# Kernel optimization log

Hardware: AMD Instinct MI355X
Metric: run time of the kernel (lower is better)

Reference implementation:

```python
import jax, jax.numpy as jnp
import numpy as np

NUM_HEADS = 16
HEAD_SIZE = 64
N_EMBD = 1024
BLOCK_SIZE = 2048
B, T = 4, 2048


def setup_inputs() -> dict:
    key = jax.random.key(0)
    ks = jax.random.split(key, 6)
    scale = (N_EMBD * NUM_HEADS) ** (-0.5)
    x = jax.random.normal(ks[0], (B, T, N_EMBD), dtype=jnp.float32)
    Wk = jax.random.normal(ks[1], (NUM_HEADS, N_EMBD, HEAD_SIZE), dtype=jnp.float32) * scale
    Wq = jax.random.normal(ks[2], (NUM_HEADS, N_EMBD, HEAD_SIZE), dtype=jnp.float32) * scale
    Wv = jax.random.normal(ks[3], (NUM_HEADS, N_EMBD, HEAD_SIZE), dtype=jnp.float32) * scale
    proj_w = jax.random.normal(ks[4], (N_EMBD, N_EMBD), dtype=jnp.float32) * (N_EMBD ** -0.5)
    proj_b = jax.random.normal(ks[5], (N_EMBD,), dtype=jnp.float32) * 0.01
    return {"x": x, "Wk": Wk, "Wq": Wq, "Wv": Wv, "proj_w": proj_w, "proj_b": proj_b}


def reference(x, Wk, Wq, Wv, proj_w, proj_b):
    Bsz, Tlen, C = x.shape
    # per-head projections: x [b,t,c] @ W [h,c,d] -> [b,h,t,d]
    q = jnp.einsum('btc,hcd->bhtd', x, Wq)
    k = jnp.einsum('btc,hcd->bhtd', x, Wk)
    v = jnp.einsum('btc,hcd->bhtd', x, Wv)
    wei = jnp.einsum('bhtd,bhsd->bhts', q, k) * (HEAD_SIZE ** -0.5)
    causal = jnp.tril(jnp.ones((Tlen, Tlen), dtype=bool))  # [T,T]
    wei = jnp.where(causal[None, None, :, :], wei, -jnp.inf)
    wei = jax.nn.softmax(wei, axis=-1)
    out = jnp.einsum('bhts,bhsd->bhtd', wei, v)
    out = out.transpose(0, 2, 1, 3).reshape(Bsz, Tlen, NUM_HEADS * HEAD_SIZE)
    out = out @ proj_w.T + proj_b  # nn.Linear: x W^T + b
    return out
```

## Files before the change

kernel.cpp:

```cpp
#include <hip/hip_runtime.h>
#include <hip/hip_bf16.h>

#define BB 4
#define TT 2048
#define CC 1024
#define HH 16
#define DD 64
#define MM (BB * TT)
#define NN_QKV 3072

typedef __attribute__((ext_vector_type(8))) short short8;
typedef __attribute__((ext_vector_type(4))) short short4v;
typedef __attribute__((ext_vector_type(4))) int i32x4;
typedef __attribute__((ext_vector_type(4))) float f32x4;
typedef __attribute__((ext_vector_type(16))) float f32x16;

static __device__ __forceinline__ float exp2_hw(float x) {
  return __builtin_amdgcn_exp2f(x);
}

static __device__ __forceinline__ short f2bf(float f) {
  __hip_bfloat16 h = __float2bfloat16(f);
  short s;
  __builtin_memcpy(&s, &h, 2);
  return s;
}

static __device__ __forceinline__ unsigned int pack2(float a, float b) {
  unsigned int lo = (unsigned short)f2bf(a);
  unsigned int hi = (unsigned short)f2bf(b);
  return lo | (hi << 16);
}

static __device__ __forceinline__ f32x16 zero16() {
  f32x16 z;
#pragma unroll
  for (int i = 0; i < 16; ++i) z[i] = 0.f;
  return z;
}

static __device__ __forceinline__ int swzv(int d) {
  return (((d & 7) ^ ((d >> 3) & 7)) << 4);
}

static __device__ __forceinline__ void gld16(const void* g, void* l) {
  __builtin_amdgcn_global_load_lds(
      (const __attribute__((address_space(1))) unsigned int*)g,
      (__attribute__((address_space(3))) unsigned int*)l, 16, 0, 0);
}

__global__ __launch_bounds__(256) void cvt8_kernel(const float* __restrict__ in,
                                                   short* __restrict__ out, int n8) {
  int i = blockIdx.x * 256 + threadIdx.x;
  if (i >= n8) return;
  const float4 a = ((const float4*)in)[i * 2];
  const float4 b = ((const float4*)in)[i * 2 + 1];
  short8 o;
  o[0] = f2bf(a.x); o[1] = f2bf(a.y); o[2] = f2bf(a.z); o[3] = f2bf(a.w);
  o[4] = f2bf(b.x); o[5] = f2bf(b.y); o[6] = f2bf(b.z); o[7] = f2bf(b.w);
  ((short8*)out)[i] = o;
}

__global__ __launch_bounds__(256) void cvtw_kernel(
    const float* __restrict__ Wq, const float* __restrict__ Wk,
    const float* __restrict__ Wv, short* __restrict__ Wt) {
  __shared__ float tile[64][65];
  const int tid = threadIdx.x;
  const int h = blockIdx.x;
  const int c0 = blockIdx.y * 64;
  const int sel = blockIdx.z;
  const float* W = (sel == 0) ? Wq : (sel == 1) ? Wk : Wv;

#pragma unroll
  for (int it = 0; it < 16; ++it) {
    int e = it * 256 + tid;
    int cc = e >> 6, d = e & 63;
    tile[d][cc] = W[((size_t)h * CC + c0 + cc) * DD + d];
  }
  __syncthreads();
#pragma unroll
  for (int it = 0; it < 16; ++it) {
    int e = it * 256 + tid;
    int d = e >> 6, cc = e & 63;
    Wt[((size_t)((sel * 16 + h) * 64 + d)) * CC + c0 + cc] = f2bf(tile[d][cc]);
  }
}

template <int MODE>
__global__ __launch_bounds__(256) void mfma_gemm_kernel(
    const short* __restrict__ A, const short* __restrict__ Bt,
    const float* __restrict__ bias,
    __hip_bfloat16* __restrict__ Oq, __hip_bfloat16* __restrict__ Ok,
    __hip_bfloat16* __restrict__ Ov, float* __restrict__ Of) {
  __shared__ __align__(16) short Als[128 * 32];
  __shared__ __align__(16) short Bls[128 * 32];

  const int tid = threadIdx.x;
  const int w = tid >> 6, l = tid & 63;
  const int lg = l >> 4, ll = l & 15;
  const int wr = w >> 1, wc = w & 1;
  const int m0 = blockIdx.x * 128;
  const int n0 = blockIdx.y * 128;

  const int row0 = tid >> 2, kc0 = (tid & 3) * 8;
  const int row1 = (tid + 256) >> 2, kc1 = (tid & 3) * 8;

  f32x4 acc[4][4] = {};

  for (int kt = 0; kt < CC; kt += 32) {
    __syncthreads();
    gld16(A + (size_t)(m0 + row0) * CC + kt + kc0, (char*)Als + w * 1024);
    gld16(A + (size_t)(m0 + row1) * CC + kt + kc1, (char*)Als + 4096 + w * 1024);
    gld16(Bt + (size_t)(n0 + row0) * CC + kt + kc0, (char*)Bls + w * 1024);
    gld16(Bt + (size_t)(n0 + row1) * CC + kt + kc1, (char*)Bls + 4096 + w * 1024);
    __syncthreads();

    short8 af[4], bfr[4];
#pragma unroll
    for (int i = 0; i < 4; ++i)
      af[i] = *(const short8*)&Als[(wr * 64 + i * 16 + ll) * 32 + lg * 8];
#pragma unroll
    for (int j = 0; j < 4; ++j)
      bfr[j] = *(const short8*)&Bls[(wc * 64 + j * 16 + ll) * 32 + lg * 8];
#pragma unroll
    for (int i = 0; i < 4; ++i)
#pragma unroll
      for (int j = 0; j < 4; ++j)
        acc[i][j] = __builtin_amdgcn_mfma_f32_16x16x32_bf16(af[i], bfr[j], acc[i][j], 0, 0, 0);
  }

  if (MODE == 0) {
    const int b = m0 >> 11;
#pragma unroll
    for (int j = 0; j < 4; ++j) {
      const int nbase = n0 + wc * 64 + j * 16;
      const int sel = nbase >> 10;
      const int h = (nbase >> 6) & 15;
      const int d = (nbase & 63) + ll;
      __hip_bfloat16* O = (sel == 0) ? Oq : (sel == 1) ? Ok : Ov;
      const float sc = (sel == 0) ? 0.18033688011112042f : 1.0f;
#pragma unroll
      for (int i = 0; i < 4; ++i) {
#pragma unroll
        for (int r = 0; r < 4; ++r) {
          const int t = (m0 + wr * 64 + i * 16 + lg * 4 + r) & (TT - 1);
          O[(((size_t)b * HH + h) * TT + t) * DD + d] = __float2bfloat16(acc[i][j][r] * sc);
        }
      }
    }
  } else {
#pragma unroll
    for (int j = 0; j < 4; ++j) {
      const int n = n0 + wc * 64 + j * 16 + ll;
      const float bv = bias[n];
#pragma unroll
      for (int i = 0; i < 4; ++i) {
#pragma unroll
        for (int r = 0; r < 4; ++r) {
          const int m = m0 + wr * 64 + i * 16 + lg * 4 + r;
          Of[(size_t)m * CC + n] = acc[i][j][r] + bv;
        }
      }
    }
  }
}

__global__ __launch_bounds__(512) void attn32_kernel(
    const __hip_bfloat16* __restrict__ qg, const __hip_bfloat16* __restrict__ kg,
    const __hip_bfloat16* __restrict__ vg, __hip_bfloat16* __restrict__ att) {
  __shared__ __align__(16) char Ks[2 * 64 * 128];
  __shared__ __align__(16) char Vt[2 * 64 * 128];

  const int tid = threadIdx.x;
  const int w = tid >> 6, l = tid & 63;
  const int l31 = l & 31, hi = l >> 5;
  const int h = blockIdx.y, b = blockIdx.z;
  const size_t base = ((size_t)b * HH + h) * TT * DD;

  const int w4 = w & 3;
  const int qt = (w >> 2) ? (int)blockIdx.x : (15 - (int)blockIdx.x);
  const int q0w = qt * 128 + w4 * 32;
  const int myq = q0w + l31;

  const short* Kg = (const short*)kg + base;
  const short* Vg = (const short*)vg + base;
  const int kr = tid >> 3;
  const int kc = tid & 7;
  const int vs = tid >> 3;
  const int vd0 = (tid & 7) * 8;

  const short* Qp = (const short*)qg + base + (size_t)myq * DD;
  const short8 qf0 = *(const short8*)(Qp + 0 + hi * 8);
  const short8 qf1 = *(const short8*)(Qp + 16 + hi * 8);
  const short8 qf2 = *(const short8*)(Qp + 32 + hi * 8);
  const short8 qf3 = *(const short8*)(Qp + 48 + hi * 8);

  f32x16 o0 = zero16(), o1 = zero16();
  float lsum = 0.f;

  const int NT = 2 * (15 - (int)blockIdx.x) + 2;
  int cur = 0;

  {
    gld16(Kg + (size_t)kr * DD + ((kc ^ (kr & 7)) * 8), Ks + w * 1024);
    const short8 va = *(const short8*)(Vg + (size_t)vs * DD + vd0);
#pragma unroll
    for (int e = 0; e < 8; ++e) {
      const int d = vd0 + e;
      *(short*)(Vt + d * 128 + ((vs * 2) ^ swzv(d))) = va[e];
    }
    __syncthreads();
  }

#pragma unroll 1
  for (int t = 0; t < NT; ++t) {
    const int sb = t * 64;
    const int nxt = cur ^ 1;
    const bool haveNext = (t + 1 < NT);

    short8 nva = {};
    if (haveNext) {
      const int sb2 = sb + 64;
      gld16(Kg + (size_t)(sb2 + kr) * DD + ((kc ^ (kr & 7)) * 8),
            Ks + nxt * 8192 + w * 1024);
      nva = *(const short8*)(Vg + (size_t)(sb2 + vs) * DD + vd0);
    }

    if (sb <= q0w + 31) {
      const char* Ksb = Ks + cur * 8192;
      const char* Vtb = Vt + cur * 8192;
#pragma unroll
      for (int ks = 0; ks < 2; ++ks) {
        const int sbh = sb + ks * 32;
        if (sbh > q0w + 31) continue;

        const int krow = ks * 32 + l31;
        const char* Kr = Ksb + krow * 128;
        const int rsz = (krow & 7) << 4;
        const short8 kf0 = *(const short8*)(Kr + ((0 * 32 + hi * 16) ^ rsz));
        const short8 kf1 = *(const short8*)(Kr + ((1 * 32 + hi * 16) ^ rsz));
        const short8 kf2 = *(const short8*)(Kr + ((2 * 32 + hi * 16) ^ rsz));
        const short8 kf3 = *(const short8*)(Kr + ((3 * 32 + hi * 16) ^ rsz));
        f32x16 sT = zero16();
        __builtin_amdgcn_s_setprio(1);
        sT = __builtin_amdgcn_mfma_f32_32x32x16_bf16(kf0, qf0, sT, 0, 0, 0);
        sT = __builtin_amdgcn_mfma_f32_32x32x16_bf16(kf1, qf1, sT, 0, 0, 0);
        sT = __builtin_amdgcn_mfma_f32_32x32x16_bf16(kf2, qf2, sT, 0, 0, 0);
        sT = __builtin_amdgcn_mfma_f32_32x32x16_bf16(kf3, qf3, sT, 0, 0, 0);
        __builtin_amdgcn_s_setprio(0);

        float p[16];
        if (sbh == q0w) {
#pragma unroll
          for (int r = 0; r < 16; ++r) {
            const int sg = sbh + (r & 3) + 8 * (r >> 2) + 4 * hi;
            p[r] = (sg > myq) ? -INFINITY : sT[r];
          }
        } else {
#pragma unroll
          for (int r = 0; r < 16; ++r) p[r] = sT[r];
        }

        float ps = 0.f;
#pragma unroll
        for (int r = 0; r < 16; ++r) {
          p[r] = exp2_hw(p[r]);
          ps += p[r];
        }
        lsum += ps;

        unsigned int W[4][2], X[4][2];
#pragma unroll
        for (int qd = 0; qd < 4; ++qd) {
          W[qd][0] = pack2(p[4 * qd + 0], p[4 * qd + 1]);
          W[qd][1] = pack2(p[4 * qd + 2], p[4 * qd + 3]);
          X[qd][0] = __shfl_xor((int)W[qd][0], 32);
          X[qd][1] = __shfl_xor((int)W[qd][1], 32);
        }

#pragma unroll
        for (int kst = 0; kst < 2; ++kst) {
          union { i32x4 i; short8 s; } A;
          A.i[0] = hi ? (int)X[2 * kst + 1][0] : (int)W[2 * kst][0];
          A.i[1] = hi ? (int)X[2 * kst + 1][1] : (int)W[2 * kst][1];
          A.i[2] = hi ? (int)W[2 * kst + 1][0] : (int)X[2 * kst][0];
          A.i[3] = hi ? (int)W[2 * kst + 1][1] : (int)X[2 * kst][1];
          const int kb = (ks * 32 + kst * 16 + hi * 8) * 2;
          const int r0 = l31, r1 = 32 + l31;
          const short8 vf0 = *(const short8*)(Vtb + r0 * 128 + (kb ^ swzv(r0)));
          const short8 vf1 = *(const short8*)(Vtb + r1 * 128 + (kb ^ swzv(r1)));
          __builtin_amdgcn_s_setprio(1);
          o0 = __builtin_amdgcn_mfma_f32_32x32x16_bf16(vf0, A.s, o0, 0, 0, 0);
          o1 = __builtin_amdgcn_mfma_f32_32x32x16_bf16(vf1, A.s, o1, 0, 0, 0);
          __builtin_amdgcn_s_setprio(0);
        }
      }
    }

    if (haveNext) {
      char* Vb = Vt + nxt * 8192;
#pragma unroll
      for (int e = 0; e < 8; ++e) {
        const int d = vd0 + e;
        *(short*)(Vb + d * 128 + ((vs * 2) ^ swzv(d))) = nva[e];
      }
    }
    __syncthreads();
    cur = nxt;
  }

  lsum += __shfl_xor(lsum, 32);
  const float inv = 1.0f / lsum;
  short* orow = (short*)att + ((size_t)b * TT + myq) * CC + h * DD;
#pragma unroll
  for (int j = 0; j < 4; ++j) {
    short4v s0, s1;
#pragma unroll
    for (int i = 0; i < 4; ++i) {
      s0[i] = f2bf(o0[4 * j + i] * inv);
      s1[i] = f2bf(o1[4 * j + i] * inv);
    }
    *(short4v*)(orow + 8 * j + 4 * hi) = s0;
    *(short4v*)(orow + 32 + 8 * j + 4 * hi) = s1;
  }
}

extern "C" void kernel_launch(void* const* d_in, const int* in_sizes, int n_in,
                              void* d_out, int out_size, void* d_ws, size_t ws_size,
                              hipStream_t stream) {
  const float* x  = (const float*)d_in[0];
  const float* Wk = (const float*)d_in[1];
  const float* Wq = (const float*)d_in[2];
  const float* Wv = (const float*)d_in[3];
  const float* pw = (const float*)d_in[4];
  const float* pb = (const float*)d_in[5];
  float* out = (float*)d_out;

  const size_t QE = (size_t)BB * HH * TT * DD;
  __hip_bfloat16* q   = (__hip_bfloat16*)d_ws;
  __hip_bfloat16* k   = q + QE;
  __hip_bfloat16* v   = k + QE;
  short* xbf          = (short*)(v + QE);
  __hip_bfloat16* att = (__hip_bfloat16*)xbf;
  short* Wt           = xbf + QE;
  short* pwbf         = Wt;

  cvt8_kernel<<<(MM * CC / 8 + 255) / 256, 256, 0, stream>>>(x, xbf, MM * CC / 8);
  cvtw_kernel<<<dim3(HH, CC / 64, 3), 256, 0, stream>>>(Wq, Wk, Wv, Wt);
  mfma_gemm_kernel<0><<<dim3(MM / 128, NN_QKV / 128), 256, 0, stream>>>(
      xbf, Wt, nullptr, q, k, v, nullptr);
  attn32_kernel<<<dim3(8, HH, BB), 512, 0, stream>>>(q, k, v, att);
  cvt8_kernel<<<(CC * CC / 8 + 255) / 256, 256, 0, stream>>>(pw, pwbf, CC * CC / 8);
  mfma_gemm_kernel<1><<<dim3(MM / 128, CC / 128), 256, 0, stream>>>(
      (const short*)att, pwbf, pb, nullptr, nullptr, nullptr, out);
}
```

Before: 168.9 us.

## Remap attention grid for XCD locality and batch both QK^T halves per tile

The 3D attention grid becomes a flat 1D grid whose block index is decoded so that all blocks of one (batch, head) land on the same XCD, improving L2 reuse of K/V. The inner loop now issues both 32-row QK^T MFMA chains together before the softmax and PV steps, instead of one 32-row half at a time, giving more independent MFMA work to overlap. Masking is handled per half with a flag, replacing the per-half skip; fully-masked halves are still computed, which is wasted work on diagonal tiles. The launch bounds now request 4 waves per EU, which may constrain registers and cause spills given the larger live set.

```diff
diff --git a/kernel.cpp b/kernel.cpp
--- a/kernel.cpp
+++ b/kernel.cpp
@@ -165,7 +165,7 @@
   }
 }
 
-__global__ __launch_bounds__(512) void attn32_kernel(
+__global__ __launch_bounds__(512, 4) void attn32_kernel(
     const __hip_bfloat16* __restrict__ qg, const __hip_bfloat16* __restrict__ kg,
     const __hip_bfloat16* __restrict__ vg, __hip_bfloat16* __restrict__ att) {
   __shared__ __align__(16) char Ks[2 * 64 * 128];
@@ -174,11 +174,17 @@
   const int tid = threadIdx.x;
   const int w = tid >> 6, l = tid & 63;
   const int l31 = l & 31, hi = l >> 5;
-  const int h = blockIdx.y, b = blockIdx.z;
+
+  const int flat = blockIdx.x;
+  const int xcd = flat & 7;
+  const int t3 = flat >> 3;
+  const int bx = t3 & 7;
+  const int hb = xcd + 8 * (t3 >> 3);
+  const int h = hb & 15, b = hb >> 4;
   const size_t base = ((size_t)b * HH + h) * TT * DD;
 
   const int w4 = w & 3;
-  const int qt = (w >> 2) ? (int)blockIdx.x : (15 - (int)blockIdx.x);
+  const int qt = (w >> 2) ? bx : (15 - bx);
   const int q0w = qt * 128 + w4 * 32;
   const int myq = q0w + l31;
 
@@ -198,7 +204,7 @@
   f32x16 o0 = zero16(), o1 = zero16();
   float lsum = 0.f;
 
-  const int NT = 2 * (15 - (int)blockIdx.x) + 2;
+  const int NT = 2 * (15 - bx) + 2;
   int cur = 0;
 
   {
@@ -229,62 +235,83 @@
     if (sb <= q0w + 31) {
       const char* Ksb = Ks + cur * 8192;
       const char* Vtb = Vt + cur * 8192;
+
+      const int kr0 = l31, kr1 = 32 + l31;
+      const char* Kp0 = Ksb + kr0 * 128;
+      const char* Kp1 = Ksb + kr1 * 128;
+      const int rs0 = (kr0 & 7) << 4;
+      const int rs1 = (kr1 & 7) << 4;
+      const short8 k0f0 = *(const short8*)(Kp0 + ((0 * 32 + hi * 16) ^ rs0));
+      const short8 k0f1 = *(const short8*)(Kp0 + ((1 * 32 + hi * 16) ^ rs0));
+      const short8 k0f2 = *(const short8*)(Kp0 + ((2 * 32 + hi * 16) ^ rs0));
+      const short8 k0f3 = *(const short8*)(Kp0 + ((3 * 32 + hi * 16) ^ rs0));
+      const short8 k1f0 = *(const short8*)(Kp1 + ((0 * 32 + hi * 16) ^ rs1));
+      const short8 k1f1 = *(const short8*)(Kp1 + ((1 * 32 + hi * 16) ^ rs1));
+      const short8 k1f2 = *(const short8*)(Kp1 + ((2 * 32 + hi * 16) ^ rs1));
+      const short8 k1f3 = *(const short8*)(Kp1 + ((3 * 32 + hi * 16) ^ rs1));
+      f32x16 sT0 = zero16(), sT1 = zero16();
+      __builtin_amdgcn_s_setprio(1);
+      sT0 = __builtin_amdgcn_mfma_f32_32x32x16_bf16(k0f0, qf0, sT0, 0, 0, 0);
+      sT0 = __builtin_amdgcn_mfma_f32_32x32x16_bf16(k0f1, qf1, sT0, 0, 0, 0);
+      sT0 = __builtin_amdgcn_mfma_f32_32x32x16_bf16(k0f2, qf2, sT0, 0, 0, 0);
+      sT0 = __builtin_amdgcn_mfma_f32_32x32x16_bf16(k0f3, qf3, sT0, 0, 0, 0);
+      sT1 = __builtin_amdgcn_mfma_f32_32x32x16_bf16(k1f0, qf0, sT1, 0, 0, 0);
+      sT1 = __builtin_amdgcn_mfma_f32_32x32x16_bf16(k1f1, qf1, sT1, 0, 0, 0);
+      sT1 = __builtin_amdgcn_mfma_f32_32x32x16_bf16(k1f2, qf2, sT1, 0, 0, 0);
+      sT1 = __builtin_amdgcn_mfma_f32_32x32x16_bf16(k1f3, qf3, sT1, 0, 0, 0);
+      __builtin_amdgcn_s_setprio(0);
+
+      const bool mk0 = (sb >= q0w);
+      const bool mk1 = (sb + 32 >= q0w);
+      const int thr = myq - 4 * hi;
+      float ps = 0.f;
+#pragma unroll
+      for (int r = 0; r < 16; ++r) {
+        float v = sT0[r];
+        if (mk0) v = (sb + (r & 3) + 8 * (r >> 2) > thr) ? -INFINITY : v;
+        v = exp2_hw(v);
+        ps += v;
+        sT0[r] = v;
+      }
+#pragma unroll
+      for (int r = 0; r < 16; ++r) {
+        float v = sT1[r];
+        if (mk1) v = (sb + 32 + (r & 3) + 8 * (r >> 2) > thr) ? -INFINITY : v;
+        v = exp2_hw(v);
+        ps += v;
+        sT1[r] = v;
+      }
+      lsum += ps;
+
+      unsigned int W0[4][2], X0[4][2], W1[4][2], X1[4][2];
+#pragma unroll
+      for (int qd = 0; qd < 4; ++qd) {
+        W0[qd][0] = pack2(sT0[4 * qd + 0], sT0[4 * qd + 1]);
+        W0[qd][1] = pack2(sT0[4 * qd + 2], sT0[4 * qd + 3]);
+        X0[qd][0] = __shfl_xor((int)W0[qd][0], 32);
+        X0[qd][1] = __shfl_xor((int)W0[qd][1], 32);
+        W1[qd][0] = pack2(sT1[4 * qd + 0], sT1[4 * qd + 1]);
+        W1[qd][1] = pack2(sT1[4 * qd + 2], sT1[4 * qd + 3]);
+        X1[qd][0] = __shfl_xor((int)W1[qd][0], 32);
+        X1[qd][1] = __shfl_xor((int)W1[qd][1], 32);
+      }
+
 #pragma unroll
       for (int ks = 0; ks < 2; ++ks) {
-        const int sbh = sb + ks * 32;
-        if (sbh > q0w + 31) continue;
-
-        const int krow = ks * 32 + l31;
-        const char* Kr = Ksb + krow * 128;
-        const int rsz = (krow & 7) << 4;
-        const short8 kf0 = *(const short8*)(Kr + ((0 * 32 + hi * 16) ^ rsz));
-        const short8 kf1 = *(const short8*)(Kr + ((1 * 32 + hi * 16) ^ rsz));
-        const short8 kf2 = *(const short8*)(Kr + ((2 * 32 + hi * 16) ^ rsz));
-        const short8 kf3 = *(const short8*)(Kr + ((3 * 32 + hi * 16) ^ rsz));
-        f32x16 sT = zero16();
-        __builtin_amdgcn_s_setprio(1);
-        sT = __builtin_amdgcn_mfma_f32_32x32x16_bf16(kf0, qf0, sT, 0, 0, 0);
-        sT = __builtin_amdgcn_mfma_f32_32x32x16_bf16(kf1, qf1, sT, 0, 0, 0);
-        sT = __builtin_amdgcn_mfma_f32_32x32x16_bf16(kf2, qf2, sT, 0, 0, 0);
-        sT = __builtin_amdgcn_mfma_f32_32x32x16_bf16(kf3, qf3, sT, 0, 0, 0);
-        __builtin_amdgcn_s_setprio(0);
-
-        float p[16];
-        if (sbh == q0w) {
-#pragma unroll
-          for (int r = 0; r < 16; ++r) {
-            const int sg = sbh + (r & 3) + 8 * (r >> 2) + 4 * hi;
-            p[r] = (sg > myq) ? -INFINITY : sT[r];
-          }
-        } else {
-#pragma unroll
-          for (int r = 0; r < 16; ++r) p[r] = sT[r];
-        }
-
-        float ps = 0.f;
-#pragma unroll
-        for (int r = 0; r < 16; ++r) {
-          p[r] = exp2_hw(p[r]);
-          ps += p[r];
-        }
-        lsum += ps;
-
-        unsigned int W[4][2], X[4][2];
-#pragma unroll
-        for (int qd = 0; qd < 4; ++qd) {
-          W[qd][0] = pack2(p[4 * qd + 0], p[4 * qd + 1]);
-          W[qd][1] = pack2(p[4 * qd + 2], p[4 * qd + 3]);
-          X[qd][0] = __shfl_xor((int)W[qd][0], 32);
-          X[qd][1] = __shfl_xor((int)W[qd][1], 32);
-        }
-
 #pragma unroll
         for (int kst = 0; kst < 2; ++kst) {
           union { i32x4 i; short8 s; } A;
-          A.i[0] = hi ? (int)X[2 * kst + 1][0] : (int)W[2 * kst][0];
-          A.i[1] = hi ? (int)X[2 * kst + 1][1] : (int)W[2 * kst][1];
-          A.i[2] = hi ? (int)W[2 * kst + 1][0] : (int)X[2 * kst][0];
-          A.i[3] = hi ? (int)W[2 * kst + 1][1] : (int)X[2 * kst][1];
+          if (ks == 0) {
+            A.i[0] = hi ? (int)X0[2 * kst + 1][0] : (int)W0[2 * kst][0];
+            A.i[1] = hi ? (int)X0[2 * kst + 1][1] : (int)W0[2 * kst][1];
+            A.i[2] = hi ? (int)W0[2 * kst + 1][0] : (int)X0[2 * kst][0];
+            A.i[3] = hi ? (int)W0[2 * kst + 1][1] : (int)X0[2 * kst][1];
+          } else {
+            A.i[0] = hi ? (int)X1[2 * kst + 1][0] : (int)W1[2 * kst][0];
+            A.i[1] = hi ? (int)X1[2 * kst + 1][1] : (int)W1[2 * kst][1];
+            A.i[2] = hi ? (int)W1[2 * kst + 1][0] : (int)X1[2 * kst][0];
+            A.i[3] = hi ? (int)W1[2 * kst + 1][1] : (int)X1[2 * kst][1];
+          }
           const int kb = (ks * 32 + kst * 16 + hi * 8) * 2;
           const int r0 = l31, r1 = 32 + l31;
           const short8 vf0 = *(const short8*)(Vtb + r0 * 128 + (kb ^ swzv(r0)));
@@ -349,7 +376,7 @@
   cvtw_kernel<<<dim3(HH, CC / 64, 3), 256, 0, stream>>>(Wq, Wk, Wv, Wt);
   mfma_gemm_kernel<0><<<dim3(MM / 128, NN_QKV / 128), 256, 0, stream>>>(
       xbf, Wt, nullptr, q, k, v, nullptr);
-  attn32_kernel<<<dim3(8, HH, BB), 512, 0, stream>>>(q, k, v, att);
+  attn32_kernel<<<dim3(512, 1, 1), 512, 0, stream>>>(q, k, v, att);
   cvt8_kernel<<<(CC * CC / 8 + 255) / 256, 256, 0, stream>>>(pw, pwbf, CC * CC / 8);
   mfma_gemm_kernel<1><<<dim3(MM / 128, CC / 128), 256, 0, stream>>>(
       (const short*)att, pwbf, pb, nullptr, nullptr, nullptr, out);
```

After: 184.4 us. 9.2% more time.

## Split attention KV range across wave groups per query tile and combine in LDS

Applied to the files above, without the earlier changes.

The attention kernel now gives each block a single 128-row query tile instead of pairing two tiles across the two 4-wave groups. Both groups work on the same queries but take alternate 64-key halves of each 128-key step, and their partial outputs and row sums are added through LDS at the end. The grid is flattened to 1024 blocks with a heavy/light ordering of query tiles for load balance. In exchange, the K/V double-buffer prefetch is removed (load then sync each step), there are extra end-of-kernel LDS reductions and barriers, and wasted masked work may rise on diagonal tiles.

```diff
diff --git a/kernel.cpp b/kernel.cpp
--- a/kernel.cpp
+++ b/kernel.cpp
@@ -168,17 +168,24 @@
 __global__ __launch_bounds__(512) void attn32_kernel(
     const __hip_bfloat16* __restrict__ qg, const __hip_bfloat16* __restrict__ kg,
     const __hip_bfloat16* __restrict__ vg, __hip_bfloat16* __restrict__ att) {
-  __shared__ __align__(16) char Ks[2 * 64 * 128];
-  __shared__ __align__(16) char Vt[2 * 64 * 128];
+  __shared__ __align__(16) char LDS[34816];
+  char* Ks = LDS;
+  char* Vt0 = LDS + 16384;
+  char* Vt1 = LDS + 24576;
 
   const int tid = threadIdx.x;
   const int w = tid >> 6, l = tid & 63;
   const int l31 = l & 31, hi = l >> 5;
-  const int h = blockIdx.y, b = blockIdx.z;
+  const int w4 = w & 3, g = w >> 2;
+
+  const int flat = blockIdx.x;
+  const int r_ = flat >> 6;
+  const int qt = (r_ < 4) ? (15 - r_) : (r_ < 8) ? (r_ + 4)
+               : (r_ < 12) ? (15 - r_) : (r_ - 12);
+  const int hb = flat & 63;
+  const int h = hb & 15, b = hb >> 4;
   const size_t base = ((size_t)b * HH + h) * TT * DD;
 
-  const int w4 = w & 3;
-  const int qt = (w >> 2) ? (int)blockIdx.x : (15 - (int)blockIdx.x);
   const int q0w = qt * 128 + w4 * 32;
   const int myq = q0w + l31;
 
@@ -198,130 +205,135 @@
   f32x16 o0 = zero16(), o1 = zero16();
   float lsum = 0.f;
 
-  const int NT = 2 * (15 - (int)blockIdx.x) + 2;
-  int cur = 0;
-
-  {
-    gld16(Kg + (size_t)kr * DD + ((kc ^ (kr & 7)) * 8), Ks + w * 1024);
-    const short8 va = *(const short8*)(Vg + (size_t)vs * DD + vd0);
+  const int npair = qt + 1;
+
+#pragma unroll 1
+  for (int pt = 0; pt < npair; ++pt) {
+    const int sb = pt * 128;
+
+    gld16(Kg + (size_t)(sb + kr) * DD + ((kc ^ (kr & 7)) * 8), Ks + w * 1024);
+    gld16(Kg + (size_t)(sb + kr + 64) * DD + ((kc ^ (kr & 7)) * 8),
+          Ks + 8192 + w * 1024);
+    const short8 va = *(const short8*)(Vg + (size_t)(sb + vs) * DD + vd0);
+    const short8 vb = *(const short8*)(Vg + (size_t)(sb + 64 + vs) * DD + vd0);
 #pragma unroll
     for (int e = 0; e < 8; ++e) {
       const int d = vd0 + e;
-      *(short*)(Vt + d * 128 + ((vs * 2) ^ swzv(d))) = va[e];
+      *(short*)(Vt0 + d * 128 + ((vs * 2) ^ swzv(d))) = va[e];
+      *(short*)(Vt1 + d * 128 + ((vs * 2) ^ swzv(d))) = vb[e];
     }
     __syncthreads();
-  }
-
-#pragma unroll 1
-  for (int t = 0; t < NT; ++t) {
-    const int sb = t * 64;
-    const int nxt = cur ^ 1;
-    const bool haveNext = (t + 1 < NT);
-
-    short8 nva = {};
-    if (haveNext) {
-      const int sb2 = sb + 64;
-      gld16(Kg + (size_t)(sb2 + kr) * DD + ((kc ^ (kr & 7)) * 8),
-            Ks + nxt * 8192 + w * 1024);
-      nva = *(const short8*)(Vg + (size_t)(sb2 + vs) * DD + vd0);
-    }
-
-    if (sb <= q0w + 31) {
-      const char* Ksb = Ks + cur * 8192;
-      const char* Vtb = Vt + cur * 8192;
-#pragma unroll
-      for (int ks = 0; ks < 2; ++ks) {
-        const int sbh = sb + ks * 32;
-        if (sbh > q0w + 31) continue;
-
-        const int krow = ks * 32 + l31;
-        const char* Kr = Ksb + krow * 128;
-        const int rsz = (krow & 7) << 4;
-        const short8 kf0 = *(const short8*)(Kr + ((0 * 32 + hi * 16) ^ rsz));
-        const short8 kf1 = *(const short8*)(Kr + ((1 * 32 + hi * 16) ^ rsz));
-        const short8 kf2 = *(const short8*)(Kr + ((2 * 32 + hi * 16) ^ rsz));
-        const short8 kf3 = *(const short8*)(Kr + ((3 * 32 + hi * 16) ^ rsz));
-        f32x16 sT = zero16();
+
+    const int sbg = sb + g * 64;
+    const char* Vtg = g ? Vt1 : Vt0;
+#pragma unroll
+    for (int ks = 0; ks < 2; ++ks) {
+      const int sbh = sbg + ks * 32;
+      if (sbh > q0w + 31) continue;
+
+      const int krow = g * 64 + ks * 32 + l31;
+      const char* Kr = Ks + krow * 128;
+      const int rsz = (krow & 7) << 4;
+      const short8 kf0 = *(const short8*)(Kr + ((0 * 32 + hi * 16) ^ rsz));
+      const short8 kf1 = *(const short8*)(Kr + ((1 * 32 + hi * 16) ^ rsz));
+      const short8 kf2 = *(const short8*)(Kr + ((2 * 32 + hi * 16) ^ rsz));
+      const short8 kf3 = *(const short8*)(Kr + ((3 * 32 + hi * 16) ^ rsz));
+      f32x16 sT = zero16();
+      __builtin_amdgcn_s_setprio(1);
+      sT = __builtin_amdgcn_mfma_f32_32x32x16_bf16(kf0, qf0, sT, 0, 0, 0);
+      sT = __builtin_amdgcn_mfma_f32_32x32x16_bf16(kf1, qf1, sT, 0, 0, 0);
+      sT = __builtin_amdgcn_mfma_f32_32x32x16_bf16(kf2, qf2, sT, 0, 0, 0);
+      sT = __builtin_amdgcn_mfma_f32_32x32x16_bf16(kf3, qf3, sT, 0, 0, 0);
+      __builtin_amdgcn_s_setprio(0);
+
+      float p[16];
+      if (sbh == q0w) {
+#pragma unroll
+        for (int r = 0; r < 16; ++r) {
+          const int sg = sbh + (r & 3) + 8 * (r >> 2) + 4 * hi;
+          p[r] = (sg > myq) ? -INFINITY : sT[r];
+        }
+      } else {
+#pragma unroll
+        for (int r = 0; r < 16; ++r) p[r] = sT[r];
+      }
+
+      float ps = 0.f;
+#pragma unroll
+      for (int r = 0; r < 16; ++r) {
+        p[r] = exp2_hw(p[r]);
+        ps += p[r];
+      }
+      lsum += ps;
+
+      unsigned int W[4][2], X[4][2];
+#pragma unroll
+      for (int qd = 0; qd < 4; ++qd) {
+        W[qd][0] = pack2(p[4 * qd + 0], p[4 * qd + 1]);
+        W[qd][1] = pack2(p[4 * qd + 2], p[4 * qd + 3]);
+        X[qd][0] = __shfl_xor((int)W[qd][0], 32);
+        X[qd][1] = __shfl_xor((int)W[qd][1], 32);
+      }
+
+#pragma unroll
+      for (int kst = 0; kst < 2; ++kst) {
+        union { i32x4 i; short8 s; } A;
+        A.i[0] = hi ? (int)X[2 * kst + 1][0] : (int)W[2 * kst][0];
+        A.i[1] = hi ? (int)X[2 * kst + 1][1] : (int)W[2 * kst][1];
+        A.i[2] = hi ? (int)W[2 * kst + 1][0] : (int)X[2 * kst][0];
+        A.i[3] = hi ? (int)W[2 * kst + 1][1] : (int)X[2 * kst][1];
+        const int kb = (ks * 32 + kst * 16 + hi * 8) * 2;
+        const int r0 = l31, r1 = 32 + l31;
+        const short8 vf0 = *(const short8*)(Vtg + r0 * 128 + (kb ^ swzv(r0)));
+        const short8 vf1 = *(const short8*)(Vtg + r1 * 128 + (kb ^ swzv(r1)));
         __builtin_amdgcn_s_setprio(1);
-        sT = __builtin_amdgcn_mfma_f32_32x32x16_bf16(kf0, qf0, sT, 0, 0, 0);
-        sT = __builtin_amdgcn_mfma_f32_32x32x16_bf16(kf1, qf1, sT, 0, 0, 0);
-        sT = __builtin_amdgcn_mfma_f32_32x32x16_bf16(kf2, qf2, sT, 0, 0, 0);
-        sT = __builtin_amdgcn_mfma_f32_32x32x16_bf16(kf3, qf3, sT, 0, 0, 0);
+        o0 = __builtin_amdgcn_mfma_f32_32x32x16_bf16(vf0, A.s, o0, 0, 0, 0);
+        o1 = __builtin_amdgcn_mfma_f32_32x32x16_bf16(vf1, A.s, o1, 0, 0, 0);
         __builtin_amdgcn_s_setprio(0);
-
-        float p[16];
-        if (sbh == q0w) {
-#pragma unroll
-          for (int r = 0; r < 16; ++r) {
-            const int sg = sbh + (r & 3) + 8 * (r >> 2) + 4 * hi;
-            p[r] = (sg > myq) ? -INFINITY : sT[r];
-          }
-        } else {
-#pragma unroll
-          for (int r = 0; r < 16; ++r) p[r] = sT[r];
-        }
-
-        float ps = 0.f;
-#pragma unroll
-        for (int r = 0; r < 16; ++r) {
-          p[r] = exp2_hw(p[r]);
-          ps += p[r];
-        }
-        lsum += ps;
-
-        unsigned int W[4][2], X[4][2];
-#pragma unroll
-        for (int qd = 0; qd < 4; ++qd) {
-          W[qd][0] = pack2(p[4 * qd + 0], p[4 * qd + 1]);
-          W[qd][1] = pack2(p[4 * qd + 2], p[4 * qd + 3]);
-          X[qd][0] = __shfl_xor((int)W[qd][0], 32);
-          X[qd][1] = __shfl_xor((int)W[qd][1], 32);
-        }
-
-#pragma unroll
-        for (int kst = 0; kst < 2; ++kst) {
-          union { i32x4 i; short8 s; } A;
-          A.i[0] = hi ? (int)X[2 * kst + 1][0] : (int)W[2 * kst][0];
-          A.i[1] = hi ? (int)X[2 * kst + 1][1] : (int)W[2 * kst][1];
-          A.i[2] = hi ? (int)W[2 * kst + 1][0] : (int)X[2 * kst][0];
-          A.i[3] = hi ? (int)W[2 * kst + 1][1] : (int)X[2 * kst][1];
-          const int kb = (ks * 32 + kst * 16 + hi * 8) * 2;
-          const int r0 = l31, r1 = 32 + l31;
-          const short8 vf0 = *(const short8*)(Vtb + r0 * 128 + (kb ^ swzv(r0)));
-          const short8 vf1 = *(const short8*)(Vtb + r1 * 128 + (kb ^ swzv(r1)));
-          __builtin_amdgcn_s_setprio(1);
-          o0 = __builtin_amdgcn_mfma_f32_32x32x16_bf16(vf0, A.s, o0, 0, 0, 0);
-          o1 = __builtin_amdgcn_mfma_f32_32x32x16_bf16(vf1, A.s, o1, 0, 0, 0);
-          __builtin_amdgcn_s_setprio(0);
-        }
-      }
-    }
-
-    if (haveNext) {
-      char* Vb = Vt + nxt * 8192;
-#pragma unroll
-      for (int e = 0; e < 8; ++e) {
-        const int d = vd0 + e;
-        *(short*)(Vb + d * 128 + ((vs * 2) ^ swzv(d))) = nva[e];
       }
     }
     __syncthreads();
-    cur = nxt;
   }
 
   lsum += __shfl_xor(lsum, 32);
-  const float inv = 1.0f / lsum;
-  short* orow = (short*)att + ((size_t)b * TT + myq) * CC + h * DD;
-#pragma unroll
-  for (int j = 0; j < 4; ++j) {
-    short4v s0, s1;
-#pragma unroll
-    for (int i = 0; i < 4; ++i) {
-      s0[i] = f2bf(o0[4 * j + i] * inv);
-      s1[i] = f2bf(o1[4 * j + i] * inv);
-    }
-    *(short4v*)(orow + 8 * j + 4 * hi) = s0;
-    *(short4v*)(orow + 32 + 8 * j + 4 * hi) = s1;
+
+  float* comb = (float*)LDS;
+  const int idx17 = (w4 * 64 + l) * 17;
+  if (g == 1) {
+#pragma unroll
+    for (int i = 0; i < 16; ++i) comb[idx17 + i] = o0[i];
+    comb[idx17 + 16] = lsum;
+  }
+  __syncthreads();
+  if (g == 0) {
+#pragma unroll
+    for (int i = 0; i < 16; ++i) o0[i] += comb[idx17 + i];
+    lsum += comb[idx17 + 16];
+  }
+  __syncthreads();
+  const int idx16 = (w4 * 64 + l) * 16;
+  if (g == 1) {
+#pragma unroll
+    for (int i = 0; i < 16; ++i) comb[idx16 + i] = o1[i];
+  }
+  __syncthreads();
+  if (g == 0) {
+#pragma unroll
+    for (int i = 0; i < 16; ++i) o1[i] += comb[idx16 + i];
+
+    const float inv = 1.0f / lsum;
+    short* orow = (short*)att + ((size_t)b * TT + myq) * CC + h * DD;
+#pragma unroll
+    for (int j = 0; j < 4; ++j) {
+      short4v s0, s1;
+#pragma unroll
+      for (int i = 0; i < 4; ++i) {
+        s0[i] = f2bf(o0[4 * j + i] * inv);
+        s1[i] = f2bf(o1[4 * j + i] * inv);
+      }
+      *(short4v*)(orow + 8 * j + 4 * hi) = s0;
+      *(short4v*)(orow + 32 + 8 * j + 4 * hi) = s1;
+    }
   }
 }
 
@@ -349,7 +361,7 @@
   cvtw_kernel<<<dim3(HH, CC / 64, 3), 256, 0, stream>>>(Wq, Wk, Wv, Wt);
   mfma_gemm_kernel<0><<<dim3(MM / 128, NN_QKV / 128), 256, 0, stream>>>(
       xbf, Wt, nullptr, q, k, v, nullptr);
-  attn32_kernel<<<dim3(8, HH, BB), 512, 0, stream>>>(q, k, v, att);
+  attn32_kernel<<<dim3(1024, 1, 1), 512, 0, stream>>>(q, k, v, att);
   cvt8_kernel<<<(CC * CC / 8 + 255) / 256, 256, 0, stream>>>(pw, pwbf, CC * CC / 8);
   mfma_gemm_kernel<1><<<dim3(MM / 128, CC / 128), 256, 0, stream>>>(
       (const short*)att, pwbf, pb, nullptr, nullptr, nullptr, out);
```

Result: faster. 163.5 us (-3.2%).
